# Kernel tuning notes

Measured on AMD Instinct MI355X. Metric: run time of the kernel, lower is better.

## Reference

```python
import jax, jax.numpy as jnp
import numpy as np

N = 20000      # nodes
E = 80000      # edges (before self loops)
NG = 64        # graphs in batch
EMB = 780      # embedding_size (768 text + 12 time)
NEG_SLOPE = 0.2
BN_EPS = 1e-5


def setup_inputs() -> dict:
    key = jax.random.key(0)
    ks = jax.random.split(key, 20)
    def rn(k, shape, s=0.05):
        return jax.random.normal(k, shape, dtype=jnp.float32) * s
    z = lambda n: jnp.zeros((n,), dtype=jnp.float32)
    o = lambda n: jnp.ones((n,), dtype=jnp.float32)
    x = jax.random.normal(ks[0], (N, 772), dtype=jnp.float32)
    edge_index = jax.random.randint(ks[1], (2, E), 0, N)
    batch = jnp.sort(jax.random.randint(ks[2], (N,), 0, NG))
    return dict(
        x=x, edge_index=edge_index, batch=batch,
        time_W=rn(ks[3], (4, 12)), time_b=z(12),
        lin_W0=rn(ks[4], (EMB, 3 * EMB)), att_src0=rn(ks[5], (3, EMB)), att_dst0=rn(ks[6], (3, EMB)),
        bias0=z(3 * EMB), gamma0=o(3 * EMB), beta0=z(3 * EMB),
        lin_W1=rn(ks[7], (3 * EMB, 3 * EMB)), att_src1=rn(ks[8], (3, EMB)), att_dst1=rn(ks[9], (3, EMB)),
        bias1=z(3 * EMB), gamma1=o(3 * EMB), beta1=z(3 * EMB),
        lin_W2=rn(ks[10], (3 * EMB, EMB)), att_src2=rn(ks[11], (1, EMB)), att_dst2=rn(ks[12], (1, EMB)),
        bias2=z(EMB), gamma2=o(EMB), beta2=z(EMB),
        mlp_W1=rn(ks[13], (EMB, 128)), mlp_b1=z(128),
        mlp_W2=rn(ks[14], (128, 64)), mlp_b2=z(64),
    )


def _gat_layer(h, src, dst, W, a_src, a_dst, b, heads):
    # PyG GATConv (eval mode: dropout off), concat=True, self loops already in src/dst
    C = W.shape[1] // heads
    hp = (h @ W).reshape(N, heads, C)                       # [N,H,C]
    a_s = jnp.sum(hp * a_src[None], axis=-1)                # [N,H]
    a_d = jnp.sum(hp * a_dst[None], axis=-1)                # [N,H]
    e = jax.nn.leaky_relu(a_s[src] + a_d[dst], NEG_SLOPE)   # [E+N,H]
    m = jax.ops.segment_max(e, dst, num_segments=N)         # segment softmax over incoming edges
    m = jnp.where(jnp.isfinite(m), m, 0.0)
    p = jnp.exp(e - m[dst])
    denom = jax.ops.segment_sum(p, dst, num_segments=N)
    alpha = p / (denom[dst] + 1e-16)                        # [E+N,H]
    out = jax.ops.segment_sum(alpha[:, :, None] * hp[src], dst, num_segments=N)  # [N,H,C]
    return out.reshape(N, heads * C) + b


def _bn(h, gamma, beta):
    # BatchNorm in training-mode math (batch statistics, biased variance)
    mu = jnp.mean(h, axis=0)
    var = jnp.mean((h - mu) ** 2, axis=0)
    return (h - mu) * jax.lax.rsqrt(var + BN_EPS) * gamma + beta


def reference(x, edge_index, batch, time_W, time_b,
              lin_W0, att_src0, att_dst0, bias0, gamma0, beta0,
              lin_W1, att_src1, att_dst1, bias1, gamma1, beta1,
              lin_W2, att_src2, att_dst2, bias2, gamma2, beta2,
              mlp_W1, mlp_b1, mlp_W2, mlp_b2):
    te = x[:, 768:772] @ time_W + time_b
    h = jnp.concatenate([jax.lax.stop_gradient(x[:, :768]), te,
                         jax.lax.stop_gradient(x[:, 772:])], axis=-1)  # [N, 780]
    sl = jnp.arange(N)
    src = jnp.concatenate([edge_index[0], sl])   # add self loops
    dst = jnp.concatenate([edge_index[1], sl])
    layers = [
        (lin_W0, att_src0, att_dst0, bias0, gamma0, beta0, 3),
        (lin_W1, att_src1, att_dst1, bias1, gamma1, beta1, 3),
        (lin_W2, att_src2, att_dst2, bias2, gamma2, beta2, 1),
    ]
    for W, a_s, a_d, b, g, bt, heads in layers:
        h = jnp.tanh(_gat_layer(h, src, dst, W, a_s, a_d, b, heads))
        h = _bn(h, g, bt)
    cnt = jax.ops.segment_sum(jnp.ones((N,), dtype=h.dtype), batch, num_segments=NG)
    pooled = jax.ops.segment_sum(h, batch, num_segments=NG) / jnp.maximum(cnt, 1.0)[:, None]
    pooled = jax.nn.relu(pooled)
    out = jnp.tanh(pooled @ mlp_W1 + mlp_b1) @ mlp_W2 + mlp_b2
    return out  # [NG, 64]
```

## Files before the change

kernel.cpp:

```cpp
#include <hip/hip_runtime.h>
#include <math.h>

#define NN   20000
#define EE   80000
#define ELP  100000
#define NGR  64
#define EMB  780
#define W3   2340
#define EMBP 832
#define W3P  2368
#define NZ   (W3+8)

static inline int cdiv_i(long long a, long long b){ return (int)((a + b - 1) / b); }

typedef _Float16 f16;
typedef _Float16 f16x4 __attribute__((ext_vector_type(4)));
typedef _Float16 f16x8 __attribute__((ext_vector_type(8)));
typedef float    f32x4 __attribute__((ext_vector_type(4)));

__device__ __forceinline__ void async_ld16(const f16* g, f16* l){
    __builtin_amdgcn_global_load_lds(
        (const __attribute__((address_space(1))) unsigned int*)g,
        (__attribute__((address_space(3))) unsigned int*)l,
        16, 0, 0);
}

__global__ void k_zero_f32(float* p, int n){
    int i = blockIdx.x*256 + threadIdx.x; if (i < n) p[i] = 0.f;
}
__global__ void k_zero_i32(int* p, int n){
    int i = blockIdx.x*256 + threadIdx.x; if (i < n) p[i] = 0;
}

__global__ void k_transpose(const float* __restrict__ W, f16* __restrict__ Wt,
                            const float* __restrict__ sc, const float* __restrict__ sh,
                            float* __restrict__ dvec, int K, int N, int KP){
    __shared__ float T[32][33];
    __shared__ float D[8][33];
    int n0 = blockIdx.x*32, k0 = blockIdx.y*32;
    int tx = threadIdx.x, ty = threadIdx.y;
    float raw[4];
#pragma unroll
    for (int r = 0; r < 4; r++){
        int k = k0 + ty + r*8;
        float w = 0.f;
        if (k < K && n0 + tx < N) w = W[(size_t)k*N + n0 + tx];
        raw[r] = w;
        T[ty + r*8][tx] = sc ? w * ((k < K) ? sc[k] : 0.f) : w;
    }
    if (sh){
        float p = 0.f;
#pragma unroll
        for (int r = 0; r < 4; r++){
            int k = k0 + ty + r*8;
            if (k < K) p += sh[k] * raw[r];
        }
        D[ty][tx] = p;
    }
    __syncthreads();
#pragma unroll
    for (int r = 0; r < 4; r++){
        int n = n0 + ty + r*8;
        int k = k0 + tx;
        if (n < N && k < KP) Wt[(size_t)n*KP + k] = (f16)T[tx][ty + r*8];
    }
    if (sh && ty == 0 && n0 + tx < N){
        float s = 0.f;
#pragma unroll
        for (int j = 0; j < 8; j++) s += D[j][tx];
        atomicAdd(&dvec[n0 + tx], s);
    }
}

__global__ void k_wvec(const float* __restrict__ W, const float* __restrict__ asrc,
                       const float* __restrict__ adst, const float* __restrict__ sc,
                       f16* __restrict__ Wt, float* __restrict__ dvec,
                       int K, int N, int KP, int H){
    int k = blockIdx.x*4 + (threadIdx.x >> 6);
    int lane = threadIdx.x & 63;
    if (k < K){
        const float* row = W + (size_t)k*N;
        float acc[6];
#pragma unroll
        for (int i = 0; i < 6; i++) acc[i] = 0.f;
        for (int c = lane; c < EMB; c += 64){
            for (int h = 0; h < H; h++){
                float wv = row[h*EMB + c];
                acc[h]     += wv * asrc[h*EMB + c];
                acc[H + h] += wv * adst[h*EMB + c];
            }
        }
        float s = sc ? sc[k] : 1.f;
        for (int i = 0; i < 2*H; i++){
            float v = acc[i];
#pragma unroll
            for (int off = 32; off; off >>= 1) v += __shfl_xor(v, off);
            if (lane == 0) Wt[(size_t)(N + i)*KP + k] = (f16)(v * s);
        }
    }
    if (blockIdx.x == 0){
        int wv = threadIdx.x >> 6;
        for (int i = wv; i < 2*H; i += 4){
            int h = (i < H) ? i : (i - H);
            const float* att = (i < H) ? (asrc + h*EMB) : (adst + h*EMB);
            float s = 0.f;
            for (int c = lane; c < EMB; c += 64) s += dvec[h*EMB + c] * att[c];
#pragma unroll
            for (int off = 32; off; off >>= 1) s += __shfl_xor(s, off);
            if (lane == 0) dvec[N + i] = s;
        }
    }
}

__global__ void k_build_h(const float* __restrict__ x, const float* __restrict__ tW,
                          const float* __restrict__ tb, f16* __restrict__ h){
    int idx = blockIdx.x*256 + threadIdx.x;
    int total = NN*(EMBP/4);
    if (idx >= total) return;
    int n = idx / (EMBP/4);
    int c0 = (idx - n*(EMBP/4))*4;
    const float* xr = x + (size_t)n*772;
    f16x4 o;
#pragma unroll
    for (int j = 0; j < 4; j++){
        int c = c0 + j; float v;
        if (c < 768) v = xr[c];
        else if (c < EMB){
            int t = c - 768;
            v = tb[t] + xr[768]*tW[t] + xr[769]*tW[12+t] + xr[770]*tW[24+t] + xr[771]*tW[36+t];
        } else v = 0.f;
        o[j] = (f16)v;
    }
    *(f16x4*)(h + (size_t)n*EMBP + c0) = o;
}

__global__ void k_deg(const int* __restrict__ ei, int* __restrict__ deg){
    int k = blockIdx.x*256 + threadIdx.x; if (k >= ELP) return;
    int d = (k < EE) ? ei[EE + k] : (k - EE);
    atomicAdd(&deg[d], 1);
}

__global__ __launch_bounds__(1024) void k_scan(int* __restrict__ deg, int* __restrict__ rp){
    __shared__ int part[1024];
    int tid = threadIdx.x;
    int i0 = tid*20;
    int n = (i0 < NN) ? min(20, NN - i0) : 0;
    int s = 0;
    for (int k = 0; k < n; k++) s += deg[i0+k];
    part[tid] = s; __syncthreads();
    for (int off = 1; off < 1024; off <<= 1){
        int t = (tid >= off) ? part[tid-off] : 0;
        __syncthreads();
        part[tid] += t;
        __syncthreads();
    }
    int run = part[tid] - s;
    for (int k = 0; k < n; k++){
        int d = deg[i0+k];
        rp[i0+k] = run;
        deg[i0+k] = run;
        run += d;
    }
    if (tid == 1023) rp[NN] = part[1023];
}

__global__ void k_fill(const int* __restrict__ ei, int* __restrict__ cursor, int* __restrict__ csrc){
    int k = blockIdx.x*256 + threadIdx.x; if (k >= ELP) return;
    int s, d;
    if (k < EE){ s = ei[k]; d = ei[EE + k]; } else { s = k - EE; d = s; }
    int pos = atomicAdd(&cursor[d], 1);
    csrc[pos] = s;
}

__global__ void k_grp(const int* __restrict__ batch, int* __restrict__ grp){
    int g = blockIdx.x*256 + threadIdx.x; if (g > NGR) return;
    int lo = 0, hi = NN;
    while (lo < hi){ int mid = (lo+hi)>>1; if (batch[mid] < g) lo = mid+1; else hi = mid; }
    grp[g] = lo;
}

__global__ __launch_bounds__(512, 4) void k_gemmT(const f16* __restrict__ A,
                                                  const f16* __restrict__ Bt,
                                                  const float* __restrict__ dvec,
                                                  f16* __restrict__ C,
                                                  float* __restrict__ a_sd,
                                                  int M, int N, int NB, int H,
                                                  int KP, int SN, int Mtiles, int NT){
    __shared__ f16 smem[36864];
    f16* sB = smem + 12288;

    int nwg = Mtiles*NT;
    int bid = blockIdx.x;
    int q = nwg >> 3, r = nwg & 7, xcd = bid & 7, lin = bid >> 3;
    int wg = (xcd < r ? xcd*(q+1) : r*(q+1) + (xcd - r)*q) + lin;
    int mt = wg / NT, nt = wg - mt*NT;
    int m0 = mt*128, n0 = nt*256;

    int tid = threadIdx.x;
    int w = tid >> 6, lane = tid & 63;
    int lm = lane & 15, lq = lane >> 4;
    int wm = w >> 2, wn = w & 3;

    int kqs = ((lane & 3) ^ ((lane >> 3) & 3)) * 8;
    const f16* gA0 = A  + (size_t)min(m0 + w*16 + (lane >> 2), M-1)*KP + kqs;
    const f16* gB0 = Bt + (size_t)min(n0 + w*32 + (lane >> 2), NB-1)*KP + kqs;
    const f16* gB1 = Bt + (size_t)min(n0 + w*32 + 16 + (lane >> 2), NB-1)*KP + kqs;
    int sa0 = w*512;
    int sb0 = w*1024, sb1 = w*1024 + 512;

    int swz  = (lq ^ ((lm >> 1) & 3)) * 8;
    int aoff = (wm*64 + lm)*32 + swz;
    int boff = (wn*64 + lm)*32 + swz;

    f32x4 acc[4][4];
#pragma unroll
    for (int i = 0; i < 4; i++)
#pragma unroll
        for (int j = 0; j < 4; j++) acc[i][j] = (f32x4)0.f;

    int KT = KP >> 5;

    async_ld16(gA0,      &smem[sa0]);
    async_ld16(gB0,      &sB[sb0]);
    async_ld16(gB1,      &sB[sb1]);
    async_ld16(gA0 + 32, &smem[4096 + sa0]);
    async_ld16(gB0 + 32, &sB[8192 + sb0]);
    async_ld16(gB1 + 32, &sB[8192 + sb1]);
    asm volatile("s_waitcnt vmcnt(3)" ::: "memory");
    __builtin_amdgcn_s_barrier();

    int cur = 0, nx2 = 2;
    for (int t = 0; t < KT; t++){
        int ac = cur*4096, bc = cur*8192;
        f16x8 aF[4], bF[4];
#pragma unroll
        for (int i = 0; i < 4; i++) aF[i] = *(const f16x8*)&smem[ac + aoff + i*512];
#pragma unroll
        for (int i = 0; i < 4; i++) bF[i] = *(const f16x8*)&sB[bc + boff + i*512];
        bool s2 = (t+2 < KT);
        if (s2){
            int ko2 = (t+2)*32;
            int a2 = nx2*4096, b2 = nx2*8192;
            async_ld16(gA0 + ko2, &smem[a2 + sa0]);
            async_ld16(gB0 + ko2, &sB[b2 + sb0]);
            async_ld16(gB1 + ko2, &sB[b2 + sb1]);
        }
        __builtin_amdgcn_s_setprio(1);
#pragma unroll
        for (int i = 0; i < 4; i++)
#pragma unroll
            for (int j = 0; j < 4; j++)
                acc[i][j] = __builtin_amdgcn_mfma_f32_16x16x32_f16(aF[i], bF[j], acc[i][j], 0, 0, 0);
        __builtin_amdgcn_s_setprio(0);
        if (s2) asm volatile("s_waitcnt vmcnt(3)" ::: "memory");
        else    asm volatile("s_waitcnt vmcnt(0)" ::: "memory");
        __builtin_amdgcn_s_barrier();
        cur = (cur == 2) ? 0 : cur + 1;
        nx2 = (nx2 == 2) ? 0 : nx2 + 1;
    }

#pragma unroll
    for (int mi = 0; mi < 4; mi++){
#pragma unroll
        for (int ni = 0; ni < 4; ni++){
            int col = n0 + wn*64 + ni*16 + lm;
            if (col >= N && col < NB){
                int jc = col - N;
                int idx = (jc < H) ? jc : (3 + jc - H);
                float dv = dvec[col];
                int rbase = m0 + wm*64 + mi*16 + lq*4;
#pragma unroll
                for (int rr = 0; rr < 4; rr++){
                    int row = rbase + rr;
                    if (row < M) a_sd[(size_t)row*6 + idx] = acc[mi][ni][rr] + dv;
                }
            }
        }
    }

    float dv4[4];
#pragma unroll
    for (int ni = 0; ni < 4; ni++){
        int gcol = n0 + wn*64 + ni*16 + lm;
        dv4[ni] = (gcol < N) ? dvec[gcol] : 0.f;
    }
    int ncols = min(256, N - n0);
#pragma unroll
    for (int mi = 0; mi < 4; mi++){
#pragma unroll
        for (int ni = 0; ni < 4; ni++){
            int colL = wn*64 + ni*16 + lm;
#pragma unroll
            for (int rr = 0; rr < 4; rr++){
                int rowL = wm*64 + mi*16 + lq*4 + rr;
                smem[rowL*264 + colL] = (f16)(acc[mi][ni][rr] + dv4[ni]);
            }
        }
    }
    asm volatile("s_waitcnt lgkmcnt(0)" ::: "memory");
    __builtin_amdgcn_s_barrier();
#pragma unroll
    for (int it = 0; it < 8; it++){
        int ch = tid + it*512;
        int rowL = ch >> 5, cc = (ch & 31)*8;
        int grow = m0 + rowL;
        if (grow < M && cc < ncols){
            if (cc + 8 <= ncols){
                f16x8 v = *(f16x8*)&smem[rowL*264 + cc];
                *(f16x8*)(C + (size_t)grow*SN + n0 + cc) = v;
            } else {
                for (int jj = cc; jj < ncols; jj++)
                    C[(size_t)grow*SN + n0 + jj] = smem[rowL*264 + jj];
            }
        }
    }
}

template<int H>
__global__ __launch_bounds__(256) void k_agg2(const f16* __restrict__ hp, const int* __restrict__ rp,
                                              const int* __restrict__ csrc, const float* __restrict__ a_sd,
                                              const float* __restrict__ bias,
                                              f16* __restrict__ y, int SP, int W){
    int n = blockIdx.x, tid = threadIdx.x, lane = tid & 63;
    int beg = rp[n], deg = rp[n+1] - beg;

    float adv[H];
#pragma unroll
    for (int h = 0; h < H; h++) adv[h] = a_sd[(size_t)n*6 + 3 + h];

    float mx[H];
#pragma unroll
    for (int h = 0; h < H; h++) mx[h] = -1e30f;
    for (int base = 0; base < deg; base += 64){
        int e = base + lane;
        if (e < deg){
            int s = csrc[beg + e];
#pragma unroll
            for (int h = 0; h < H; h++){
                float t = a_sd[(size_t)s*6 + h] + adv[h];
                t = t > 0.f ? t : 0.2f*t;
                mx[h] = fmaxf(mx[h], t);
            }
        }
    }
#pragma unroll
    for (int off = 32; off; off >>= 1)
#pragma unroll
        for (int h = 0; h < H; h++) mx[h] = fmaxf(mx[h], __shfl_xor(mx[h], off));

    float dn[H];
#pragma unroll
    for (int h = 0; h < H; h++) dn[h] = 0.f;
    for (int base = 0; base < deg; base += 64){
        int e = base + lane;
        if (e < deg){
            int s = csrc[beg + e];
#pragma unroll
            for (int h = 0; h < H; h++){
                float t = a_sd[(size_t)s*6 + h] + adv[h];
                t = t > 0.f ? t : 0.2f*t;
                dn[h] += expf(t - mx[h]);
            }
        }
    }
#pragma unroll
    for (int off = 32; off; off >>= 1)
#pragma unroll
        for (int h = 0; h < H; h++) dn[h] += __shfl_xor(dn[h], off);
    float inv[H];
#pragma unroll
    for (int h = 0; h < H; h++) inv[h] = 1.f / (dn[h] + 1e-16f);

    float acc[2][8];
#pragma unroll
    for (int g = 0; g < 2; g++)
#pragma unroll
        for (int j = 0; j < 8; j++) acc[g][j] = 0.f;
    int  cg[2];  cg[0] = tid*8; cg[1] = 2048 + tid*8;
    bool act[2]; act[0] = cg[0] < W; act[1] = cg[1] < W;
    int hlo[2], hhi[2], nsp[2];
#pragma unroll
    for (int g = 0; g < 2; g++){
        int c = cg[g];
        int hl = min(c / EMB, H-1);
        int hh = min((c+7) / EMB, H-1);
        hlo[g] = hl; hhi[g] = hh;
        nsp[g] = (hh > hl) ? (EMB*(hl+1) - c) : 8;
    }

    for (int base = 0; base < deg; base += 64){
        int cnt = min(64, deg - base);
        int sl = 0; float al[H];
        {
            int e = base + lane;
            if (e < deg){
                sl = csrc[beg + e];
#pragma unroll
                for (int h = 0; h < H; h++){
                    float t = a_sd[(size_t)sl*6 + h] + adv[h];
                    t = t > 0.f ? t : 0.2f*t;
                    al[h] = expf(t - mx[h]) * inv[h];
                }
            } else {
#pragma unroll
                for (int h = 0; h < H; h++) al[h] = 0.f;
            }
        }
#pragma unroll 4
        for (int e = 0; e < cnt; e++){
            int s = __shfl(sl, e);
            float a0 = __shfl(al[0], e);
            float a1 = (H==3) ? __shfl(al[1], e) : a0;
            float a2 = (H==3) ? __shfl(al[2], e) : a0;
            const f16* row = hp + (size_t)s*SP;
#pragma unroll
            for (int g = 0; g < 2; g++){
                if (act[g]){
                    f16x8 v = *(const f16x8*)(row + cg[g]);
                    float lo = (hlo[g]==0) ? a0 : (hlo[g]==1 ? a1 : a2);
                    float hi = (hhi[g]==0) ? a0 : (hhi[g]==1 ? a1 : a2);
#pragma unroll
                    for (int j = 0; j < 8; j++){
                        float alj = (j < nsp[g]) ? lo : hi;
                        acc[g][j] += alj * (float)v[j];
                    }
                }
            }
        }
    }

#pragma unroll
    for (int g = 0; g < 2; g++){
        int c = cg[g];
        if (c < SP){
            f16x8 o;
#pragma unroll
            for (int j = 0; j < 8; j++){
                float vv = (c + j < W) ? tanhf(acc[g][j] + bias[c+j]) : 0.f;
                o[j] = (f16)vv;
            }
            *(f16x8*)(y + (size_t)n*SP + c) = o;
        }
    }
}

__global__ void k_bnstat(const f16* __restrict__ y, float* __restrict__ ps,
                         float* __restrict__ pq, int W, int SP){
    int c0 = (blockIdx.x*256 + threadIdx.x)*4;
    if (c0 >= W) return;
    int slice = blockIdx.y;
    int r0 = (int)(((long long)NN*slice)/128);
    int r1 = (int)(((long long)NN*(slice+1))/128);
    float s[4] = {0,0,0,0}, q[4] = {0,0,0,0};
    for (int r = r0; r < r1; r++){
        f16x4 u = *(const f16x4*)(y + (size_t)r*SP + c0);
#pragma unroll
        for (int j = 0; j < 4; j++){ float v = (float)u[j]; s[j] += v; q[j] += v*v; }
    }
#pragma unroll
    for (int j = 0; j < 4; j++){
        ps[(size_t)slice*W3 + c0+j] = s[j];
        pq[(size_t)slice*W3 + c0+j] = q[j];
    }
}

__global__ void k_bnfin(const float* __restrict__ ps, const float* __restrict__ pq,
                        const float* __restrict__ gamma, const float* __restrict__ beta,
                        float* __restrict__ sc, float* __restrict__ sh,
                        float* __restrict__ dvec, int W, int zn){
    int c = blockIdx.x*256 + threadIdx.x;
    if (c < W){
        float m = 0.f, q = 0.f;
        for (int s = 0; s < 128; s++){ m += ps[(size_t)s*W3 + c]; q += pq[(size_t)s*W3 + c]; }
        m *= (1.f/NN);
        float v = q * (1.f/NN) - m*m;
        float is = 1.f / sqrtf(v + 1e-5f);
        float g = gamma[c];
        sc[c] = is * g;
        sh[c] = beta[c] - m * is * g;
    }
    if (c < zn) dvec[c] = 0.f;
}

__global__ void k_pool(const f16* __restrict__ h, const int* __restrict__ grp,
                       float* __restrict__ pooled){
    int g = blockIdx.x;
    int c = threadIdx.x*4;
    if (c >= EMB) return;
    int r0 = grp[g], r1 = grp[g+1];
    float s0=0.f, s1=0.f, s2=0.f, s3=0.f;
    for (int r = r0; r < r1; r++){
        f16x4 u = *(const f16x4*)(h + (size_t)r*EMBP + c);
        s0 += (float)u[0]; s1 += (float)u[1]; s2 += (float)u[2]; s3 += (float)u[3];
    }
    pooled[g*EMB + c] = s0; pooled[g*EMB + c+1] = s1;
    pooled[g*EMB + c+2] = s2; pooled[g*EMB + c+3] = s3;
}

__global__ __launch_bounds__(256) void k_mlp(const float* __restrict__ pooled, const int* __restrict__ grp,
                                             const float* __restrict__ sc, const float* __restrict__ sh,
                                             const float* __restrict__ W1, const float* __restrict__ b1,
                                             const float* __restrict__ W2, const float* __restrict__ b2,
                                             float* __restrict__ out){
    __shared__ float p[EMB];
    __shared__ float hid[128];
    int g = blockIdx.x, tid = threadIdx.x;
    int cnt = grp[g+1] - grp[g];
    float ic = 1.f / fmaxf((float)cnt, 1.f);
    for (int c = tid; c < EMB; c += 256){
        float v = pooled[g*EMB + c] * ic * sc[c] + sh[c];
        p[c] = v > 0.f ? v : 0.f;
    }
    __syncthreads();
    if (tid < 128){
        float s = b1[tid];
        for (int k = 0; k < EMB; k++) s += p[k] * W1[k*128 + tid];
        hid[tid] = tanhf(s);
    }
    __syncthreads();
    if (tid < 64){
        float s = b2[tid];
        for (int k = 0; k < 128; k++) s += hid[k] * W2[k*64 + tid];
        out[g*64 + tid] = s;
    }
}

extern "C" void kernel_launch(void* const* d_in, const int* in_sizes, int n_in,
                              void* d_out, int out_size, void* d_ws, size_t ws_size,
                              hipStream_t stream) {
    (void)in_sizes; (void)n_in; (void)out_size;
    const float* x    = (const float*)d_in[0];
    const int*   ei   = (const int*)  d_in[1];
    const int*   batch= (const int*)  d_in[2];
    const float* tW   = (const float*)d_in[3];
    const float* tb   = (const float*)d_in[4];
    const float* W0   = (const float*)d_in[5];
    const float* as0  = (const float*)d_in[6];
    const float* ad0  = (const float*)d_in[7];
    const float* b0   = (const float*)d_in[8];
    const float* g0   = (const float*)d_in[9];
    const float* be0  = (const float*)d_in[10];
    const float* W1   = (const float*)d_in[11];
    const float* as1  = (const float*)d_in[12];
    const float* ad1  = (const float*)d_in[13];
    const float* b1   = (const float*)d_in[14];
    const float* g1   = (const float*)d_in[15];
    const float* be1  = (const float*)d_in[16];
    const float* W2   = (const float*)d_in[17];
    const float* as2  = (const float*)d_in[18];
    const float* ad2  = (const float*)d_in[19];
    const float* b2   = (const float*)d_in[20];
    const float* g2   = (const float*)d_in[21];
    const float* be2  = (const float*)d_in[22];
    const float* mW1  = (const float*)d_in[23];
    const float* mb1  = (const float*)d_in[24];
    const float* mW2  = (const float*)d_in[25];
    const float* mb2  = (const float*)d_in[26];
    float* outp = (float*)d_out;

    size_t off = 0;
    auto carve = [&](size_t bytes) -> void* {
        void* p = (char*)d_ws + off;
        off = (off + bytes + 255) & ~(size_t)255;
        return p;
    };
    f16* big1 = (f16*)carve((size_t)NN*W3P*2);
    f16* big2 = (f16*)carve((size_t)NN*W3P*2);
    f16* Wt   = (f16*)carve((size_t)NZ*W3P*2);
    float* a_sd  = (float*)carve((size_t)NN*6*4);
    float* psum  = (float*)carve((size_t)128*W3*4);
    float* psq   = (float*)carve((size_t)128*W3*4);
    float* sc    = (float*)carve((size_t)W3*4);
    float* sh    = (float*)carve((size_t)W3*4);
    float* dvec  = (float*)carve((size_t)NZ*4);
    float* pooled= (float*)carve((size_t)NGR*EMB*4);
    int*   grp   = (int*)carve((size_t)(NGR+1)*4);
    int*   deg   = (int*)carve((size_t)NN*4);
    int*   rp    = (int*)carve((size_t)(NN+1)*4);
    int*   csrc  = (int*)carve((size_t)ELP*4);

    if (ws_size < off) return;

    k_zero_i32<<<cdiv_i(NN,256),256,0,stream>>>(deg, NN);
    k_deg<<<cdiv_i(ELP,256),256,0,stream>>>(ei, deg);
    k_scan<<<1,1024,0,stream>>>(deg, rp);
    k_fill<<<cdiv_i(ELP,256),256,0,stream>>>(ei, deg, csrc);
    k_grp<<<1,256,0,stream>>>(batch, grp);

    k_build_h<<<cdiv_i((long long)NN*(EMBP/4),256),256,0,stream>>>(x, tW, tb, big1);
    k_zero_f32<<<cdiv_i(NZ,256),256,0,stream>>>(dvec, NZ);

    struct Layer { const float* W; const float* as; const float* ad; const float* b;
                   const float* g; const float* be; int H; int K; int KP; };
    Layer layers[3] = {
        {W0, as0, ad0, b0, g0, be0, 3, EMB, EMBP},
        {W1, as1, ad1, b1, g1, be1, 3, W3,  W3P },
        {W2, as2, ad2, b2, g2, be2, 1, W3,  W3P },
    };

    for (int L = 0; L < 3; L++){
        Layer& ly = layers[L];
        int Wout  = ly.H * EMB;
        int NB    = Wout + 2*ly.H;
        int SPout = (Wout == W3) ? W3P : EMBP;
        const float* scale = (L == 0) ? nullptr : sc;
        const float* shift = (L == 0) ? nullptr : sh;

        dim3 tg(cdiv_i(Wout,32), cdiv_i(ly.KP,32));
        k_transpose<<<tg, dim3(32,8), 0, stream>>>(ly.W, Wt, scale, shift, dvec, ly.K, Wout, ly.KP);
        k_wvec<<<cdiv_i(ly.K,4),256,0,stream>>>(ly.W, ly.as, ly.ad, scale, Wt, dvec, ly.K, Wout, ly.KP, ly.H);

        int Mtiles = cdiv_i(NN,128), NT = cdiv_i(NB,256);
        k_gemmT<<<Mtiles*NT, 512, 0, stream>>>(big1, Wt, dvec, big2, a_sd,
                                               NN, Wout, NB, ly.H, ly.KP, SPout, Mtiles, NT);

        if (ly.H == 3)
            k_agg2<3><<<NN,256,0,stream>>>(big2, rp, csrc, a_sd, ly.b, big1, SPout, Wout);
        else
            k_agg2<1><<<NN,256,0,stream>>>(big2, rp, csrc, a_sd, ly.b, big1, SPout, Wout);

        dim3 gs(cdiv_i(Wout/4,256), 128);
        k_bnstat<<<gs,256,0,stream>>>(big1, psum, psq, Wout, SPout);
        int zn = (L < 2) ? NZ : 0;
        k_bnfin<<<cdiv_i(Wout,256),256,0,stream>>>(psum, psq, ly.g, ly.be, sc, sh, dvec, Wout, zn);
    }

    k_pool<<<NGR,256,0,stream>>>(big1, grp, pooled);
    k_mlp<<<NGR,256,0,stream>>>(pooled, grp, sc, sh, mW1, mb1, mW2, mb2, outp);
}
```

Before: 1.427 ms.

## Assign one wavefront per node in GAT aggregation and cache first edge chunk

The aggregation kernel now maps one 64-lane wavefront to each destination node, with four nodes per 256-thread block, instead of one whole block per node. Each lane covers several 8-column groups (5 for three heads, 2 for one head). Before, all four waves in a block repeated the same softmax max and denominator passes; that duplicate work and the per-node block overhead go away. The first 64 incoming edges' source indices and attention logits are also kept in registers, so the max, sum and weighting passes do not reload them. In exchange, each lane holds more accumulator registers and does more serial gather work per node, which may reduce occupancy.

```diff
diff --git a/kernel.cpp b/kernel.cpp
--- a/kernel.cpp
+++ b/kernel.cpp
@@ -316,22 +316,39 @@
     }
 }
 
-template<int H>
-__global__ __launch_bounds__(256) void k_agg2(const f16* __restrict__ hp, const int* __restrict__ rp,
+template<int H, int NG>
+__global__ __launch_bounds__(256) void k_agg3(const f16* __restrict__ hp, const int* __restrict__ rp,
                                               const int* __restrict__ csrc, const float* __restrict__ a_sd,
                                               const float* __restrict__ bias,
                                               f16* __restrict__ y, int SP, int W){
-    int n = blockIdx.x, tid = threadIdx.x, lane = tid & 63;
+    int n = blockIdx.x*4 + (threadIdx.x >> 6);
+    if (n >= NN) return;
+    int lane = threadIdx.x & 63;
     int beg = rp[n], deg = rp[n+1] - beg;
 
     float adv[H];
 #pragma unroll
     for (int h = 0; h < H; h++) adv[h] = a_sd[(size_t)n*6 + 3 + h];
 
+    bool act0 = lane < deg;
+    int sl0 = 0;
+    float t0[H];
+    if (act0){
+        sl0 = csrc[beg + lane];
+#pragma unroll
+        for (int h = 0; h < H; h++){
+            float t = a_sd[(size_t)sl0*6 + h] + adv[h];
+            t0[h] = t > 0.f ? t : 0.2f*t;
+        }
+    } else {
+#pragma unroll
+        for (int h = 0; h < H; h++) t0[h] = -1e30f;
+    }
+
     float mx[H];
 #pragma unroll
-    for (int h = 0; h < H; h++) mx[h] = -1e30f;
-    for (int base = 0; base < deg; base += 64){
+    for (int h = 0; h < H; h++) mx[h] = t0[h];
+    for (int base = 64; base < deg; base += 64){
         int e = base + lane;
         if (e < deg){
             int s = csrc[beg + e];
@@ -350,8 +367,8 @@
 
     float dn[H];
 #pragma unroll
-    for (int h = 0; h < H; h++) dn[h] = 0.f;
-    for (int base = 0; base < deg; base += 64){
+    for (int h = 0; h < H; h++) dn[h] = act0 ? expf(t0[h] - mx[h]) : 0.f;
+    for (int base = 64; base < deg; base += 64){
         int e = base + lane;
         if (e < deg){
             int s = csrc[beg + e];
@@ -371,28 +388,35 @@
 #pragma unroll
     for (int h = 0; h < H; h++) inv[h] = 1.f / (dn[h] + 1e-16f);
 
-    float acc[2][8];
-#pragma unroll
-    for (int g = 0; g < 2; g++)
-#pragma unroll
-        for (int j = 0; j < 8; j++) acc[g][j] = 0.f;
-    int  cg[2];  cg[0] = tid*8; cg[1] = 2048 + tid*8;
-    bool act[2]; act[0] = cg[0] < W; act[1] = cg[1] < W;
-    int hlo[2], hhi[2], nsp[2];
-#pragma unroll
-    for (int g = 0; g < 2; g++){
-        int c = cg[g];
+    float acc[NG][8];
+    int  hlo[NG], hhi[NG], nsp[NG];
+    bool cok[NG];
+    int  cbase[NG];
+#pragma unroll
+    for (int g = 0; g < NG; g++){
+        int c = g*512 + lane*8;
+        cbase[g] = c;
+        cok[g] = c < SP;
         int hl = min(c / EMB, H-1);
         int hh = min((c+7) / EMB, H-1);
         hlo[g] = hl; hhi[g] = hh;
         nsp[g] = (hh > hl) ? (EMB*(hl+1) - c) : 8;
+#pragma unroll
+        for (int j = 0; j < 8; j++) acc[g][j] = 0.f;
     }
 
     for (int base = 0; base < deg; base += 64){
         int cnt = min(64, deg - base);
-        int sl = 0; float al[H];
-        {
+        int sl; float al[H];
+        if (base == 0){
+            sl = sl0;
+#pragma unroll
+            for (int h = 0; h < H; h++) al[h] = act0 ? expf(t0[h] - mx[h]) * inv[h] : 0.f;
+        } else {
             int e = base + lane;
+            sl = 0;
+#pragma unroll
+            for (int h = 0; h < H; h++) al[h] = 0.f;
             if (e < deg){
                 sl = csrc[beg + e];
 #pragma unroll
@@ -401,9 +425,6 @@
                     t = t > 0.f ? t : 0.2f*t;
                     al[h] = expf(t - mx[h]) * inv[h];
                 }
-            } else {
-#pragma unroll
-                for (int h = 0; h < H; h++) al[h] = 0.f;
             }
         }
 #pragma unroll 4
@@ -414,11 +435,11 @@
             float a2 = (H==3) ? __shfl(al[2], e) : a0;
             const f16* row = hp + (size_t)s*SP;
 #pragma unroll
-            for (int g = 0; g < 2; g++){
-                if (act[g]){
-                    f16x8 v = *(const f16x8*)(row + cg[g]);
-                    float lo = (hlo[g]==0) ? a0 : (hlo[g]==1 ? a1 : a2);
-                    float hi = (hhi[g]==0) ? a0 : (hhi[g]==1 ? a1 : a2);
+            for (int g = 0; g < NG; g++){
+                if (cok[g]){
+                    f16x8 v = *(const f16x8*)(row + cbase[g]);
+                    float lo = (H==3) ? ((hlo[g]==0) ? a0 : ((hlo[g]==1) ? a1 : a2)) : a0;
+                    float hi = (H==3) ? ((hhi[g]==0) ? a0 : ((hhi[g]==1) ? a1 : a2)) : a0;
 #pragma unroll
                     for (int j = 0; j < 8; j++){
                         float alj = (j < nsp[g]) ? lo : hi;
@@ -430,9 +451,9 @@
     }
 
 #pragma unroll
-    for (int g = 0; g < 2; g++){
-        int c = cg[g];
-        if (c < SP){
+    for (int g = 0; g < NG; g++){
+        if (cok[g]){
+            int c = cbase[g];
             f16x8 o;
 #pragma unroll
             for (int j = 0; j < 8; j++){
@@ -615,9 +636,9 @@
                                                NN, Wout, NB, ly.H, ly.KP, SPout, Mtiles, NT);
 
         if (ly.H == 3)
-            k_agg2<3><<<NN,256,0,stream>>>(big2, rp, csrc, a_sd, ly.b, big1, SPout, Wout);
+            k_agg3<3,5><<<cdiv_i(NN,4),256,0,stream>>>(big2, rp, csrc, a_sd, ly.b, big1, SPout, Wout);
         else
-            k_agg2<1><<<NN,256,0,stream>>>(big2, rp, csrc, a_sd, ly.b, big1, SPout, Wout);
+            k_agg3<1,2><<<cdiv_i(NN,4),256,0,stream>>>(big2, rp, csrc, a_sd, ly.b, big1, SPout, Wout);
 
         dim3 gs(cdiv_i(Wout/4,256), 128);
         k_bnstat<<<gs,256,0,stream>>>(big1, psum, psq, Wout, SPout);
```

After: 1.436 ms. No clear change (+0.6%).
